# Kernel tuning notes

Measured on AMD Instinct MI355X. Metric: run time of the kernel, lower is better.

## Reference

```python
import jax, jax.numpy as jnp
import numpy as np

IN, H, T, B, PRE = 168, 512, 512, 64, 168


def _lstm_dir(x_tbi, Wih, Whh, b, reverse):
    """Single-direction LSTM. x_tbi: [T,B,in]. Wih:[4H,in] Whh:[4H,H] b:[4H].
    Returns hidden states [T,B,H] in forward time order.
    PyTorch gate order: i, f, g, o."""
    Bsz = x_tbi.shape[1]
    h0 = jnp.zeros((Bsz, H), x_tbi.dtype)
    c0 = jnp.zeros((Bsz, H), x_tbi.dtype)
    WihT, WhhT = Wih.T, Whh.T

    def step(carry, xt):
        h, c = carry
        gates = xt @ WihT + h @ WhhT + b  # [B,4H]
        i, f, g, o = jnp.split(gates, 4, axis=-1)
        c = jax.nn.sigmoid(f) * c + jax.nn.sigmoid(i) * jnp.tanh(g)
        h = jax.nn.sigmoid(o) * jnp.tanh(c)
        return (h, c), h

    _, hs = jax.lax.scan(step, (h0, c0), x_tbi, reverse=reverse)
    return hs


def _bilstm_layer(x_tbi, Wih, Whh, b):
    # Wih: [2,4H,in], Whh: [2,4H,H], b: [2,4H] (b_ih+b_hh pre-summed)
    fwd = _lstm_dir(x_tbi, Wih[0], Whh[0], b[0], reverse=False)
    bwd = _lstm_dir(x_tbi, Wih[1], Whh[1], b[1], reverse=True)
    return jnp.concatenate([fwd, bwd], axis=-1)  # [T,B,2H]


def setup_inputs() -> dict:
    key = jax.random.key(0)
    ks = jax.random.split(key, 9)
    s = 1.0 / np.sqrt(H)
    u = lambda k, shp: jax.random.uniform(k, shp, jnp.float32, -s, s)
    return {
        "x": jax.random.normal(ks[0], (B, T, IN), jnp.float32),
        "Wih0": u(ks[1], (2, 4 * H, IN)),
        "Whh0": u(ks[2], (2, 4 * H, H)),
        "b0": u(ks[3], (2, 4 * H)),
        "Wih1": u(ks[4], (2, 4 * H, 2 * H)),
        "Whh1": u(ks[5], (2, 4 * H, H)),
        "b1": u(ks[6], (2, 4 * H)),
        "Wout": u(ks[7], (PRE, 2 * H)),
        "bout": u(ks[8], (PRE,)),
    }


def reference(x, Wih0, Whh0, b0, Wih1, Whh1, b1, Wout, bout):
    # batch_first: x [B,T,IN] -> scan over time [T,B,IN]
    x_tbi = jnp.swapaxes(x, 0, 1)
    h1 = _bilstm_layer(x_tbi, Wih0, Whh0, b0)      # [T,B,2H]
    h2 = _bilstm_layer(h1, Wih1, Whh1, b1)         # [T,B,2H] (dropout=eval identity)
    temp = jnp.swapaxes(h2, 0, 1)                   # [B,T,2H]
    out = temp @ Wout.T + bout                      # [B,T,PRE]
    return out
```

## Files before the change

### kernel.cpp

```cpp
#include <hip/hip_runtime.h>

typedef _Float16 f16;
typedef _Float16 f16x8 __attribute__((ext_vector_type(8)));
typedef float    f32x4 __attribute__((ext_vector_type(4)));

#define GLOAD16(gptr, lptr)                                                    \
  __builtin_amdgcn_global_load_lds(                                            \
      (const __attribute__((address_space(1))) void*)(gptr),                   \
      (__attribute__((address_space(3))) void*)(lptr), 16, 0, 0)

static __device__ __forceinline__ float sigm(float x) {
  return 1.f / (1.f + __expf(-x));
}
static __device__ __forceinline__ float tanh_f(float x) {
  return 2.f / (1.f + __expf(-2.f * x)) - 1.f;
}

#define TSEQ 512
#define BATCH 64
#define HID 512
#define INW 168
#define PREW 168
#define CHUNK 128

__global__ void k_zero_bars(int* bars) {
  bars[threadIdx.x] = 0;
}

__global__ void k_sent(float* out, float v) { out[0] = v; }

__global__ void k_conv_x(const float* __restrict__ x, f16* __restrict__ xf) {
  int cid = blockIdx.x * 256 + threadIdx.x;
  int m  = cid & 63;
  int kh = (cid >> 6) % 24;
  int t  = cid / (64 * 24);
  f16x8 o;
  if (kh < 21) {
    const float* p = x + ((size_t)m * TSEQ + t) * INW + kh * 8;
#pragma unroll
    for (int i = 0; i < 8; i++) o[i] = (f16)p[i];
  } else {
#pragma unroll
    for (int i = 0; i < 8; i++) o[i] = (f16)0.f;
  }
  *(f16x8*)(xf + (size_t)cid * 8) = o;
}

__global__ void k_conv_w(const float* __restrict__ W, f16* __restrict__ P,
                         int Nrows, int K, int KHp, int total) {
  int cid = blockIdx.x * 256 + threadIdx.x;
  if (cid >= total) return;
  int n_ = cid & 63;
  int kh = (cid >> 6) % KHp;
  int nb = cid / (64 * KHp);
  int row = nb * 64 + n_;
  f16x8 o;
#pragma unroll
  for (int i = 0; i < 8; i++) {
    int k = kh * 8 + i;
    float v = (row < Nrows && k < K) ? W[(size_t)row * K + k] : 0.f;
    o[i] = (f16)v;
  }
  *(f16x8*)(P + (size_t)cid * 8) = o;
}

__global__ __launch_bounds__(256) void k_gemm_pre(
    const f16* __restrict__ Ap, const f16* __restrict__ Bp,
    const float* __restrict__ bias, f16* __restrict__ Cpre, int KH,
    int tb0, int tb1) {
  __shared__ f16 Alds[4096];
  __shared__ f16 Blds[4096];
  __shared__ f16 Clds[128 * 128];

  int tid = threadIdx.x;
  int w = tid >> 6, lane = tid & 63, quad = lane >> 4, lc = lane & 15;
  int mh = w & 1, nh = w >> 1;
  int d = blockIdx.z;
  int tBase = d ? tb1 : tb0;
  size_t rbA0 = (size_t)tBase + blockIdx.y * 2;
  size_t nb0 = (size_t)d * 32 + blockIdx.x * 2;
  int kIters = KH >> 2;

  f32x4 acc[4][4];
#pragma unroll
  for (int a = 0; a < 4; a++)
#pragma unroll
    for (int b = 0; b < 4; b++) acc[a][b] = (f32x4){0.f, 0.f, 0.f, 0.f};

  int wv = tid >> 6;
  for (int kk = 0; kk < kIters; kk++) {
    __syncthreads();
    GLOAD16(Ap + ((rbA0 + 0) * KH + kk * 4) * 512 + tid * 8, &Alds[0    + wv * 512]);
    GLOAD16(Ap + ((rbA0 + 1) * KH + kk * 4) * 512 + tid * 8, &Alds[2048 + wv * 512]);
    GLOAD16(Bp + ((nb0 + 0) * KH + kk * 4) * 512 + tid * 8, &Blds[0    + wv * 512]);
    GLOAD16(Bp + ((nb0 + 1) * KH + kk * 4) * 512 + tid * 8, &Blds[2048 + wv * 512]);
    __syncthreads();

    f16x8 af[4], bf[4];
#pragma unroll
    for (int i = 0; i < 4; i++)
      af[i] = *(const f16x8*)&Alds[(((mh * 4 + quad) * 64) + i * 16 + lc) * 8];
#pragma unroll
    for (int i = 0; i < 4; i++)
      bf[i] = *(const f16x8*)&Blds[(((nh * 4 + quad) * 64) + i * 16 + lc) * 8];
#pragma unroll
    for (int mt = 0; mt < 4; mt++)
#pragma unroll
      for (int nt = 0; nt < 4; nt++)
        acc[mt][nt] = __builtin_amdgcn_mfma_f32_16x16x32_f16(af[mt], bf[nt],
                                                             acc[mt][nt], 0, 0, 0);
  }
  __syncthreads();

#pragma unroll
  for (int nt = 0; nt < 4; nt++) {
    int col = nh * 64 + nt * 16 + lc;
    float bv = bias[d * 2048 + blockIdx.x * 128 + col];
#pragma unroll
    for (int mt = 0; mt < 4; mt++) {
      int row0 = mh * 64 + mt * 16 + quad * 4;
#pragma unroll
      for (int r = 0; r < 4; r++)
        Clds[(row0 + r) * 128 + col] = (f16)(acc[mt][nt][r] + bv);
    }
  }
  __syncthreads();

  int row = tid >> 1, half = tid & 1;
  size_t rg = (size_t)blockIdx.y * 128 + row;
  f16* dst = Cpre + ((size_t)d * 8192 + rg) * 2048 + blockIdx.x * 128 + half * 64;
  const f16* srcl = &Clds[row * 128 + half * 64];
#pragma unroll
  for (int i = 0; i < 8; i++) *(f16x8*)(dst + i * 8) = *(const f16x8*)(srcl + i * 8);
}

__global__ __launch_bounds__(256) void k_gemm_out(
    const f16* __restrict__ Ap, const f16* __restrict__ Bp,
    const float* __restrict__ bout, float* __restrict__ out) {
  __shared__ f16 Alds[4096];
  __shared__ f16 Blds[4096];
  const int KH = 128;

  int tid = threadIdx.x;
  int w = tid >> 6, lane = tid & 63, quad = lane >> 4, lc = lane & 15;
  int mh = w & 1, nh = w >> 1;
  size_t rb0 = (size_t)blockIdx.y * 2;
  size_t nb0 = (size_t)blockIdx.x * 2;

  f32x4 acc[4][4];
#pragma unroll
  for (int a = 0; a < 4; a++)
#pragma unroll
    for (int b = 0; b < 4; b++) acc[a][b] = (f32x4){0.f, 0.f, 0.f, 0.f};

  int wv = tid >> 6;
  for (int kk = 0; kk < 32; kk++) {
    __syncthreads();
    GLOAD16(Ap + ((rb0 + 0) * KH + kk * 4) * 512 + tid * 8, &Alds[0    + wv * 512]);
    GLOAD16(Ap + ((rb0 + 1) * KH + kk * 4) * 512 + tid * 8, &Alds[2048 + wv * 512]);
    GLOAD16(Bp + ((nb0 + 0) * KH + kk * 4) * 512 + tid * 8, &Blds[0    + wv * 512]);
    GLOAD16(Bp + ((nb0 + 1) * KH + kk * 4) * 512 + tid * 8, &Blds[2048 + wv * 512]);
    __syncthreads();

    f16x8 af[4], bf[4];
#pragma unroll
    for (int i = 0; i < 4; i++)
      af[i] = *(const f16x8*)&Alds[(((mh * 4 + quad) * 64) + i * 16 + lc) * 8];
#pragma unroll
    for (int i = 0; i < 4; i++)
      bf[i] = *(const f16x8*)&Blds[(((nh * 4 + quad) * 64) + i * 16 + lc) * 8];
#pragma unroll
    for (int mt = 0; mt < 4; mt++)
#pragma unroll
      for (int nt = 0; nt < 4; nt++)
        acc[mt][nt] = __builtin_amdgcn_mfma_f32_16x16x32_f16(af[mt], bf[nt],
                                                             acc[mt][nt], 0, 0, 0);
  }

#pragma unroll
  for (int nt = 0; nt < 4; nt++) {
    int col = blockIdx.x * 128 + nh * 64 + nt * 16 + lc;
    if (col >= PREW) continue;
    float bv = bout[col];
#pragma unroll
    for (int mt = 0; mt < 4; mt++) {
      int row0 = blockIdx.y * 128 + mh * 64 + mt * 16 + quad * 4;
#pragma unroll
      for (int r = 0; r < 4; r++) {
        int rg = row0 + r;
        int t = rg >> 6, m = rg & 63;
        out[((size_t)m * TSEQ + t) * PREW + col] = acc[mt][nt][r] + bv;
      }
    }
  }
}

__global__ __launch_bounds__(256, 1) void k_lstm(
    const f16* __restrict__ pre, const f16* __restrict__ WhhP,
    f16* __restrict__ hbuf, int* bars, float* __restrict__ cbuf, int s0) {
  __shared__ f16 hlds[64 * 64 * 8];
  __shared__ float glds[4 * 32 * 64];

  int tid = threadIdx.x;
  int lane = tid & 63, quad = lane >> 4, lc = lane & 15;
  int blk = blockIdx.x;
  int d = blk >> 4, wg = blk & 15;
  int j0 = wg * 32;
  int g = tid >> 6;

  f16x8 wf[16][2];
#pragma unroll
  for (int ki = 0; ki < 16; ki++)
#pragma unroll
    for (int nt = 0; nt < 2; nt++) {
      int col = g * HID + j0 + nt * 16 + lc;
      size_t nb = (size_t)d * 32 + (col >> 6);
      int n_ = col & 63;
      wf[ki][nt] = *(const f16x8*)&WhhP[((nb * 64 + ki * 4 + quad) * 64 + n_) * 8];
    }

  int m_ep = tid >> 2, jg = tid & 3;
  float* cp = cbuf + ((size_t)(d * 16 + wg) * 256 + tid) * 8;
  float cst[8];
  if (s0 == 0) {
#pragma unroll
    for (int i = 0; i < 8; i++) cst[i] = 0.f;
  } else {
#pragma unroll
    for (int i = 0; i < 8; i++) cst[i] = cp[i];
  }
  int* bar = bars + d * 64;

  for (int s = s0; s < s0 + CHUNK; s++) {
    int t = d ? (TSEQ - 1 - s) : s;

    const f16* pp = pre + (((size_t)d * 128 + (t & 127)) * 64 + m_ep) * 2048 + j0 + jg * 8;
    f16x8 pi = *(const f16x8*)(pp + 0 * HID);
    f16x8 pf = *(const f16x8*)(pp + 1 * HID);
    f16x8 pg = *(const f16x8*)(pp + 2 * HID);
    f16x8 po = *(const f16x8*)(pp + 3 * HID);

    f32x4 acc[4][2];
#pragma unroll
    for (int a = 0; a < 4; a++)
#pragma unroll
      for (int b = 0; b < 2; b++) acc[a][b] = (f32x4){0.f, 0.f, 0.f, 0.f};

    if (s > 0) {
      int tp = d ? t + 1 : t - 1;
      while (__hip_atomic_load(bar, __ATOMIC_RELAXED, __HIP_MEMORY_SCOPE_AGENT) < 64 * s) {}

      const f16* src = hbuf + ((size_t)tp * 128 + d * 64) * 512 + tid * 8;
      f32x4 tmp[16];
#pragma unroll
      for (int it = 0; it < 16; it++) {
        const f16* p = src + it * 2048;
        asm volatile("global_load_dwordx4 %0, %1, off sc0 sc1"
                     : "=v"(tmp[it]) : "v"(p) : "memory");
      }
      asm volatile("s_waitcnt vmcnt(0)" ::: "memory");
#pragma unroll
      for (int it = 0; it < 16; it++)
        *(f32x4*)&hlds[it * 2048 + tid * 8] = tmp[it];
      __syncthreads();

#pragma unroll
      for (int ki = 0; ki < 16; ki++) {
        f16x8 af[4];
#pragma unroll
        for (int mt = 0; mt < 4; mt++)
          af[mt] = *(const f16x8*)&hlds[(((ki * 4 + quad) * 64) + mt * 16 + lc) * 8];
#pragma unroll
        for (int mt = 0; mt < 4; mt++)
#pragma unroll
          for (int nt = 0; nt < 2; nt++)
            acc[mt][nt] = __builtin_amdgcn_mfma_f32_16x16x32_f16(af[mt], wf[ki][nt],
                                                                 acc[mt][nt], 0, 0, 0);
      }
    }

#pragma unroll
    for (int nt = 0; nt < 2; nt++)
#pragma unroll
      for (int mt = 0; mt < 4; mt++)
        *(f32x4*)&glds[((g * 32 + nt * 16 + lc) * 64) + mt * 16 + quad * 4] = acc[mt][nt];
    __syncthreads();

    f16x8 hv;
#pragma unroll
    for (int e = 0; e < 8; e++) {
      int j = jg * 8 + e;
      float gi = glds[(0 * 32 + j) * 64 + m_ep] + (float)pi[e];
      float gf = glds[(1 * 32 + j) * 64 + m_ep] + (float)pf[e];
      float gg = glds[(2 * 32 + j) * 64 + m_ep] + (float)pg[e];
      float go = glds[(3 * 32 + j) * 64 + m_ep] + (float)po[e];
      float c = sigm(gf) * cst[e] + sigm(gi) * tanh_f(gg);
      cst[e] = c;
      hv[e] = (f16)(sigm(go) * tanh_f(c));
    }
    f16* hdst = &hbuf[(((size_t)t * 128 + d * 64 + wg * 4 + jg) * 64 + m_ep) * 8];
    f32x4 hv4 = *(f32x4*)&hv;
    asm volatile("global_store_dwordx4 %0, %1, off sc0 sc1"
                 :: "v"(hdst), "v"(hv4) : "memory");
    asm volatile("s_waitcnt vmcnt(0)" ::: "memory");
    if (lane == 0)
      __hip_atomic_fetch_add(bar, 1, __ATOMIC_RELAXED, __HIP_MEMORY_SCOPE_AGENT);
  }

#pragma unroll
  for (int i = 0; i < 8; i++) cp[i] = cst[i];
}

extern "C" void kernel_launch(void* const* d_in, const int* in_sizes, int n_in,
                              void* d_out, int out_size, void* d_ws, size_t ws_size,
                              hipStream_t stream) {
  (void)in_sizes; (void)n_in; (void)out_size;
  const float* x    = (const float*)d_in[0];
  const float* Wih0 = (const float*)d_in[1];
  const float* Whh0 = (const float*)d_in[2];
  const float* b0   = (const float*)d_in[3];
  const float* Wih1 = (const float*)d_in[4];
  const float* Whh1 = (const float*)d_in[5];
  const float* b1   = (const float*)d_in[6];
  const float* Wout = (const float*)d_in[7];
  const float* bout = (const float*)d_in[8];
  float* out = (float*)d_out;
  char* ws = (char*)d_ws;

  size_t off = 0;
  auto carve = [&](size_t bytes) {
    size_t o = off; off += (bytes + 255) & ~(size_t)255; return o;
  };
  size_t o_bars  = carve(1024);
  size_t o_cbuf  = carve((size_t)2 * 16 * 256 * 8 * 4);
  size_t o_xf    = carve((size_t)512 * 24 * 512 * 2);
  size_t o_w0p   = carve((size_t)64 * 24 * 512 * 2);
  size_t o_whh0p = carve((size_t)64 * 64 * 512 * 2);
  size_t o_w1p   = carve((size_t)64 * 128 * 512 * 2);
  size_t o_whh1p = carve((size_t)64 * 64 * 512 * 2);
  size_t o_woutp = carve((size_t)4 * 128 * 512 * 2);
  size_t o_h1    = carve((size_t)512 * 128 * 512 * 2);
  size_t o_h2    = carve((size_t)512 * 128 * 512 * 2);
  size_t o_pre   = carve((size_t)2 * 128 * 64 * 2048 * 2);

  if (ws_size < off) {
    k_sent<<<1, 1, 0, stream>>>(out, (float)(ws_size >> 20));
    return;
  }

  int*   bars  = (int*)(ws + o_bars);
  float* cbuf  = (float*)(ws + o_cbuf);
  f16*   xf    = (f16*)(ws + o_xf);
  f16*   w0p   = (f16*)(ws + o_w0p);
  f16*   whh0p = (f16*)(ws + o_whh0p);
  f16*   w1p   = (f16*)(ws + o_w1p);
  f16*   whh1p = (f16*)(ws + o_whh1p);
  f16*   woutp = (f16*)(ws + o_woutp);
  f16*   h1    = (f16*)(ws + o_h1);
  f16*   h2    = (f16*)(ws + o_h2);
  f16*   pre   = (f16*)(ws + o_pre);

  k_zero_bars<<<1, 256, 0, stream>>>(bars);
  k_conv_x<<<3072, 256, 0, stream>>>(x, xf);
  k_conv_w<<<384,  256, 0, stream>>>(Wih0, w0p,   4096, 168,  24,  98304);
  k_conv_w<<<1024, 256, 0, stream>>>(Whh0, whh0p, 4096, 512,  64,  262144);
  k_conv_w<<<2048, 256, 0, stream>>>(Wih1, w1p,   4096, 1024, 128, 524288);
  k_conv_w<<<1024, 256, 0, stream>>>(Whh1, whh1p, 4096, 512,  64,  262144);
  k_conv_w<<<128,  256, 0, stream>>>(Wout, woutp, 168,  1024, 128, 32768);

  for (int c = 0; c < 4; c++) {
    int tb0 = 128 * c, tb1 = 384 - 128 * c;
    k_gemm_pre<<<dim3(16, 64, 2), 256, 0, stream>>>(xf, w0p, b0, pre, 24, tb0, tb1);
    k_lstm<<<32, 256, 0, stream>>>(pre, whh0p, h1, bars, cbuf, 128 * c);
  }
  for (int c = 0; c < 4; c++) {
    int tb0 = 128 * c, tb1 = 384 - 128 * c;
    k_gemm_pre<<<dim3(16, 64, 2), 256, 0, stream>>>(h1, w1p, b1, pre, 128, tb0, tb1);
    k_lstm<<<32, 256, 0, stream>>>(pre, whh1p, h2, bars + 128, cbuf, 128 * c);
  }
  k_gemm_out<<<dim3(2, 256, 1), 256, 0, stream>>>(h2, woutp, bout, out);
}
```

Measured before the change: 8.736 ms.

## Replace atomic step barrier with sentinel-filled hidden-state polling

The per-step atomic counter barrier between LSTM workgroups is removed. Before each call, the hidden-state buffers are pre-filled with a 0xFFFF NaN sentinel, and consumers re-load any 16-byte chunk that still contains the sentinel until real data arrives. This removes the store-wait, the atomic increment and the counter spin from the recurrent critical path, so readiness is signalled by the data itself. The cost is a full-buffer fill kernel on every call and repeated global loads while polling. It relies on real h values never being 0xFFFF, which holds because they come from bounded tanh outputs.

```diff
diff --git a/kernel.cpp b/kernel.cpp
--- a/kernel.cpp
+++ b/kernel.cpp
@@ -23,11 +23,17 @@
 #define PREW 168
 #define CHUNK 128
 
-__global__ void k_zero_bars(int* bars) {
-  bars[threadIdx.x] = 0;
-}
-
 __global__ void k_sent(float* out, float v) { out[0] = v; }
+
+__global__ void k_fill_ff(f16* p, long n16) {
+  long i = (long)blockIdx.x * 256 + threadIdx.x;
+  if (i >= n16) return;
+  union { f32x4 f; unsigned u[4]; } v;
+  v.u[0] = v.u[1] = v.u[2] = v.u[3] = 0xFFFFFFFFu;
+  f16* dst = p + i * 8;
+  asm volatile("global_store_dwordx4 %0, %1, off sc0 sc1"
+               :: "v"(dst), "v"(v.f) : "memory");
+}
 
 __global__ void k_conv_x(const float* __restrict__ x, f16* __restrict__ xf) {
   int cid = blockIdx.x * 256 + threadIdx.x;
@@ -197,7 +203,7 @@
 
 __global__ __launch_bounds__(256, 1) void k_lstm(
     const f16* __restrict__ pre, const f16* __restrict__ WhhP,
-    f16* __restrict__ hbuf, int* bars, float* __restrict__ cbuf, int s0) {
+    f16* __restrict__ hbuf, float* __restrict__ cbuf, int s0) {
   __shared__ f16 hlds[64 * 64 * 8];
   __shared__ float glds[4 * 32 * 64];
 
@@ -229,7 +235,6 @@
 #pragma unroll
     for (int i = 0; i < 8; i++) cst[i] = cp[i];
   }
-  int* bar = bars + d * 64;
 
   for (int s = s0; s < s0 + CHUNK; s++) {
     int t = d ? (TSEQ - 1 - s) : s;
@@ -248,20 +253,40 @@
 
     if (s > 0) {
       int tp = d ? t + 1 : t - 1;
-      while (__hip_atomic_load(bar, __ATOMIC_RELAXED, __HIP_MEMORY_SCOPE_AGENT) < 64 * s) {}
-
       const f16* src = hbuf + ((size_t)tp * 128 + d * 64) * 512 + tid * 8;
+
       f32x4 tmp[16];
+      unsigned pend = 0xFFFFu;
 #pragma unroll
       for (int it = 0; it < 16; it++) {
         const f16* p = src + it * 2048;
         asm volatile("global_load_dwordx4 %0, %1, off sc0 sc1"
                      : "=v"(tmp[it]) : "v"(p) : "memory");
       }
-      asm volatile("s_waitcnt vmcnt(0)" ::: "memory");
-#pragma unroll
-      for (int it = 0; it < 16; it++)
-        *(f32x4*)&hlds[it * 2048 + tid * 8] = tmp[it];
+      do {
+        asm volatile("s_waitcnt vmcnt(0)" ::: "memory");
+        unsigned np = 0;
+#pragma unroll
+        for (int it = 0; it < 16; it++) {
+          if (pend & (1u << it)) {
+            union { f32x4 f; unsigned u[4]; } x;
+            x.f = tmp[it];
+            bool bad = false;
+#pragma unroll
+            for (int q = 0; q < 4; q++)
+              bad |= ((x.u[q] & 0xFFFFu) == 0xFFFFu) | ((x.u[q] >> 16) == 0xFFFFu);
+            if (bad) {
+              np |= 1u << it;
+              const f16* p = src + it * 2048;
+              asm volatile("global_load_dwordx4 %0, %1, off sc0 sc1"
+                           : "=v"(tmp[it]) : "v"(p) : "memory");
+            } else {
+              *(f32x4*)&hlds[it * 2048 + tid * 8] = tmp[it];
+            }
+          }
+        }
+        pend = np;
+      } while (pend);
       __syncthreads();
 
 #pragma unroll
@@ -302,9 +327,8 @@
     f32x4 hv4 = *(f32x4*)&hv;
     asm volatile("global_store_dwordx4 %0, %1, off sc0 sc1"
                  :: "v"(hdst), "v"(hv4) : "memory");
-    asm volatile("s_waitcnt vmcnt(0)" ::: "memory");
-    if (lane == 0)
-      __hip_atomic_fetch_add(bar, 1, __ATOMIC_RELAXED, __HIP_MEMORY_SCOPE_AGENT);
+
+    __syncthreads();
   }
 
 #pragma unroll
@@ -331,7 +355,6 @@
   auto carve = [&](size_t bytes) {
     size_t o = off; off += (bytes + 255) & ~(size_t)255; return o;
   };
-  size_t o_bars  = carve(1024);
   size_t o_cbuf  = carve((size_t)2 * 16 * 256 * 8 * 4);
   size_t o_xf    = carve((size_t)512 * 24 * 512 * 2);
   size_t o_w0p   = carve((size_t)64 * 24 * 512 * 2);
@@ -348,7 +371,6 @@
     return;
   }
 
-  int*   bars  = (int*)(ws + o_bars);
   float* cbuf  = (float*)(ws + o_cbuf);
   f16*   xf    = (f16*)(ws + o_xf);
   f16*   w0p   = (f16*)(ws + o_w0p);
@@ -360,7 +382,8 @@
   f16*   h2    = (f16*)(ws + o_h2);
   f16*   pre   = (f16*)(ws + o_pre);
 
-  k_zero_bars<<<1, 256, 0, stream>>>(bars);
+  k_fill_ff<<<32768, 256, 0, stream>>>(h1, (long)8388608);
+
   k_conv_x<<<3072, 256, 0, stream>>>(x, xf);
   k_conv_w<<<384,  256, 0, stream>>>(Wih0, w0p,   4096, 168,  24,  98304);
   k_conv_w<<<1024, 256, 0, stream>>>(Whh0, whh0p, 4096, 512,  64,  262144);
@@ -371,12 +394,12 @@
   for (int c = 0; c < 4; c++) {
     int tb0 = 128 * c, tb1 = 384 - 128 * c;
     k_gemm_pre<<<dim3(16, 64, 2), 256, 0, stream>>>(xf, w0p, b0, pre, 24, tb0, tb1);
-    k_lstm<<<32, 256, 0, stream>>>(pre, whh0p, h1, bars, cbuf, 128 * c);
+    k_lstm<<<32, 256, 0, stream>>>(pre, whh0p, h1, cbuf, 128 * c);
   }
   for (int c = 0; c < 4; c++) {
     int tb0 = 128 * c, tb1 = 384 - 128 * c;
     k_gemm_pre<<<dim3(16, 64, 2), 256, 0, stream>>>(h1, w1p, b1, pre, 128, tb0, tb1);
-    k_lstm<<<32, 256, 0, stream>>>(pre, whh1p, h2, bars + 128, cbuf, 128 * c);
+    k_lstm<<<32, 256, 0, stream>>>(pre, whh1p, h2, cbuf, 128 * c);
   }
   k_gemm_out<<<dim3(2, 256, 1), 256, 0, stream>>>(h2, woutp, bout, out);
 }
```

New measurement: 7.966 ms. 8.8% less time.
